# Performance work log

Hardware: AMD Instinct MI355X
Metric: run time of the kernel (lower is better)

## Reference

```python
import jax, jax.numpy as jnp
import numpy as np

N = 50000
E = 800000
IN_FEAT = 256
HIDDEN = 256
NUM_CLASS = 10
NUM_GRAPHS = 512
LAYERS = 2


def setup_inputs() -> dict:
    key = jax.random.key(0)
    ks = jax.random.split(key, 10)
    x = jax.random.normal(ks[0], (N, IN_FEAT), dtype=jnp.float32)
    edge_index = jax.random.randint(ks[1], (2, E), 0, N, dtype=jnp.int32)
    batch = jnp.sort(jax.random.randint(ks[2], (N,), 0, NUM_GRAPHS, dtype=jnp.int32))
    s_in = 1.0 / np.sqrt(IN_FEAT)
    s_h = 1.0 / np.sqrt(HIDDEN)
    enc_W = jax.random.uniform(ks[3], (IN_FEAT, HIDDEN), jnp.float32, -s_in, s_in)
    enc_b = jax.random.uniform(ks[4], (HIDDEN,), jnp.float32, -s_in, s_in)
    conv_W = jax.random.uniform(ks[5], (LAYERS, HIDDEN, HIDDEN), jnp.float32, -s_h, s_h)
    conv_b = jax.random.uniform(ks[6], (LAYERS, HIDDEN), jnp.float32, -s_h, s_h)
    out_W = jax.random.uniform(ks[7], (HIDDEN, NUM_CLASS), jnp.float32, -s_h, s_h)
    out_b = jax.random.uniform(ks[8], (NUM_CLASS,), jnp.float32, -s_h, s_h)
    return {"x": x, "edge_index": edge_index, "batch": batch,
            "enc_W": enc_W, "enc_b": enc_b,
            "conv_W": conv_W, "conv_b": conv_b,
            "out_W": out_W, "out_b": out_b}


def _gcn_conv(x, row, col, deg_norm_edge, W, b):
    # PyG GCNConv: linear transform, then normalized scatter-add aggregation.
    h = x @ W                                   # [N, H]
    msg = h[row] * deg_norm_edge[:, None]       # [E+N, H] gather + scale
    out = jax.ops.segment_sum(msg, col, num_segments=N)  # scatter-add
    return out + b


def reference(x, edge_index, batch, enc_W, enc_b, conv_W, conv_b, out_W, out_b):
    # self-loops appended once (same structure every layer)
    loops = jnp.arange(N, dtype=edge_index.dtype)
    row = jnp.concatenate([edge_index[0], loops])  # source
    col = jnp.concatenate([edge_index[1], loops])  # target
    deg = jax.ops.segment_sum(jnp.ones_like(col, dtype=x.dtype), col, num_segments=N)
    dinv = jnp.where(deg > 0, jax.lax.rsqrt(deg), 0.0)
    norm = dinv[row] * dinv[col]                # symmetric GCN normalization per edge

    h = x @ enc_W + enc_b
    for i in range(LAYERS):
        h = jax.nn.relu(_gcn_conv(h, row, col, norm, conv_W[i], conv_b[i]))

    # global_mean_pool over `batch` segment ids
    sums = jax.ops.segment_sum(h, batch, num_segments=NUM_GRAPHS)
    cnts = jax.ops.segment_sum(jnp.ones((N,), dtype=h.dtype), batch, num_segments=NUM_GRAPHS)
    pooled = sums / jnp.maximum(cnts, 1.0)[:, None]

    # dropout is identity in eval mode
    return pooled @ out_W + out_b
```

## Files before the change

kernel.cpp:

```cpp
#include <hip/hip_runtime.h>

#define NN 50000
#define NE 800000
#define HD 256
#define NG 512
#define NC 10
#define SCAN_B ((NN + 255) / 256)
#define REP 8
#define GEMM_G ((NN + 31) / 32)
#define EDGE_G ((NE + 255) / 256)

typedef unsigned short u16;
typedef unsigned char u8;
typedef short v8s __attribute__((ext_vector_type(8)));
typedef float v4f __attribute__((ext_vector_type(4)));
typedef float v2f __attribute__((ext_vector_type(2)));
typedef u16 v4u __attribute__((ext_vector_type(4)));

static __device__ __forceinline__ float bf2f(u16 u) {
    return __uint_as_float(((unsigned)u) << 16);
}
static __device__ __forceinline__ u16 f2bf(float f) {
    unsigned u = __float_as_uint(f);
    unsigned r = (u + 0x7fffu + ((u >> 16) & 1u)) >> 16;
    return (u16)r;
}
static __device__ __forceinline__ int clampi(int v, int lo, int hi) {
    return min(max(v, lo), hi);
}
static __device__ __forceinline__ float ldf(const void* p, size_t i, int isbf) {
    return isbf ? bf2f(((const u16*)p)[i]) : ((const float*)p)[i];
}

static __device__ __forceinline__ u8 f32_to_fp8(float f) {
#if __has_builtin(__builtin_amdgcn_cvt_pk_fp8_f32)
    int r = __builtin_amdgcn_cvt_pk_fp8_f32(f, f, 0, false);
    return (u8)(r & 0xff);
#else
    float a = fabsf(f);
    unsigned s = (__float_as_uint(f) >> 31) << 7;
    if (a < 0.0009765625f) return (u8)s;
    a = fminf(a, 448.f);
    if (a < 0.015625f) {
        int m = (int)(a * 512.f + 0.5f);
        return (u8)(s | min(m, 7));
    }
    unsigned u = __float_as_uint(a);
    unsigned r = u + 0x0007FFFFu + ((u >> 20) & 1u);
    int e = (int)(r >> 23) - 127 + 7;
    if (e > 15) return (u8)(s | 0x7E);
    unsigned m = (r >> 20) & 7u;
    return (u8)(s | ((unsigned)e << 3) | m);
#endif
}
static __device__ __forceinline__ v4f fp8x4_to_f32(unsigned v) {
#if __has_builtin(__builtin_amdgcn_cvt_pk_f32_fp8)
    v2f lo = __builtin_amdgcn_cvt_pk_f32_fp8(v, false);
    v2f hi = __builtin_amdgcn_cvt_pk_f32_fp8(v, true);
    return (v4f){lo[0], lo[1], hi[0], hi[1]};
#else
    v4f o;
#pragma unroll
    for (int j = 0; j < 4; j++) {
        unsigned b = (v >> (8 * j)) & 0xffu;
        unsigned e = (b >> 3) & 15u, m = b & 7u;
        float val = e ? __uint_as_float(((e + 120u) << 23) | (m << 20))
                      : (float)m * 0.001953125f;
        o[j] = (b & 0x80u) ? -val : val;
    }
    return o;
#endif
}

__global__ void k_detect(const u16* __restrict__ xu, int* __restrict__ mode) {
    __shared__ int cnt;
    if (threadIdx.x == 0) cnt = 0;
    __syncthreads();
    int bad = 0;
    for (int i = threadIdx.x; i < 4096; i += 256) {
        float v = bf2f(xu[2 * i]);
        float av = fabsf(v);
        if (av > 100.f || (av < 1e-3f && av != 0.f)) bad++;
    }
    atomicAdd(&cnt, bad);
    __syncthreads();
    if (threadIdx.x == 0) mode[0] = (cnt > 1024) ? 0 : 1;
}

__global__ void k_prep(const void* __restrict__ enc_W, const void* __restrict__ conv_W,
                       const void* __restrict__ enc_b, const void* __restrict__ conv_b,
                       const void* __restrict__ out_b,
                       u16* __restrict__ Wp, float* __restrict__ biasf,
                       const int* __restrict__ modep) {
    int md = modep[0];
    int b = blockIdx.x;
    if (b < 768) {
        int wi = b >> 8;
        int n = b & 255, k = threadIdx.x;
        const void* W = (wi == 0) ? enc_W : conv_W;
        size_t off = (wi == 0) ? 0 : (size_t)(wi - 1) * HD * HD;
        int nt = n >> 4, m = n & 15;
        int ks = k >> 5, q = (k >> 3) & 3, j = k & 7;
        size_t idx = ((((size_t)nt * 8 + ks) * 64) + q * 16 + m) * 8 + j;
        Wp[(size_t)wi * HD * HD + idx] = f2bf(ldf(W, off + (size_t)k * HD + n, md));
    } else {
        for (int j = threadIdx.x; j < 768 + NC; j += 256) {
            float v = (j < 256) ? ldf(enc_b, j, md)
                    : (j < 768) ? ldf(conv_b, j - 256, md)
                                : ldf(out_b, j - 768, md);
            biasf[j] = v;
        }
    }
}

static __device__ __forceinline__ void edges_body(
        int i, const int* __restrict__ ecol, const int* __restrict__ batch,
        int* __restrict__ deg_r, int* __restrict__ gptr) {
    int r = (i >> 8) & (REP - 1);
    if (i < NE) atomicAdd(&deg_r[r * NN + clampi(ecol[i], 0, NN - 1)], 1);
    if (i < NN) {
        int b = clampi(batch[i], 0, NG - 1);
        int bp = (i == 0) ? -1 : clampi(batch[i - 1], 0, NG - 1);
        for (int g = bp + 1; g <= b; g++) gptr[g] = i;
        if (i == NN - 1)
            for (int g = b + 1; g <= NG; g++) gptr[g] = NN;
    }
}

static __device__ __forceinline__ void scatter_body(
        int i, const int* __restrict__ row, const int* __restrict__ col,
        const int* __restrict__ cptr, const int* __restrict__ offc,
        int* __restrict__ fill_r, int* __restrict__ csrc) {
    int r = (i >> 8) & (REP - 1);
    if (i < NE) {
        int c = clampi(col[i], 0, NN - 1);
        int rw = clampi(row[i], 0, NN - 1);
        int pos = cptr[c] + offc[r * NN + c] + atomicAdd(&fill_r[r * NN + c], 1);
        if (pos >= 0 && pos < NE) csrc[pos] = rw;
    }
}

static __device__ __forceinline__ void gemm_body(
        int bid, u16* As, const void* __restrict__ A, const u16* __restrict__ Wp,
        const float* __restrict__ biasf, const float* __restrict__ dinvp,
        void* __restrict__ out, int M, int hasBias, int outFp8, int amode) {
    int tid = threadIdx.x;
    int wave = tid >> 6;
    int lane = tid & 63;
    int row0 = bid * 32;
    if (row0 >= M) return;
    int m = lane & 15, q = lane >> 4;

#pragma unroll
    for (int it = 0; it < 4; it++) {
        int fb = it * 4 + wave;
        int mt = fb >> 3, ks = fb & 7;
        int row = min(row0 + mt * 16 + m, M - 1);
        int colE = ks * 32 + q * 8;
        v8s v;
        if (amode) {
            v = *(const v8s*)((const u16*)A + (size_t)row * HD + colE);
        } else {
            const float* af = (const float*)A + (size_t)row * HD + colE;
            v4f x0 = *(const v4f*)af;
            v4f x1 = *(const v4f*)(af + 4);
            v[0] = (short)f2bf(x0[0]); v[1] = (short)f2bf(x0[1]);
            v[2] = (short)f2bf(x0[2]); v[3] = (short)f2bf(x0[3]);
            v[4] = (short)f2bf(x1[0]); v[5] = (short)f2bf(x1[1]);
            v[6] = (short)f2bf(x1[2]); v[7] = (short)f2bf(x1[3]);
        }
        *(v8s*)&As[((size_t)fb * 64 + lane) * 8] = v;
    }
    __syncthreads();

    v4f acc[2][4];
#pragma unroll
    for (int i = 0; i < 2; i++)
#pragma unroll
        for (int j = 0; j < 4; j++) acc[i][j] = (v4f){0.f, 0.f, 0.f, 0.f};

    const u16* wp = Wp + (size_t)wave * 4 * 8 * 64 * 8;

#pragma unroll
    for (int ks = 0; ks < 8; ks++) {
        v8s bfr[4];
#pragma unroll
        for (int nt = 0; nt < 4; nt++)
            bfr[nt] = *(const v8s*)(wp + ((size_t)(nt * 8 + ks) * 64 + lane) * 8);
        v8s a[2];
#pragma unroll
        for (int mt = 0; mt < 2; mt++)
            a[mt] = *(const v8s*)&As[((size_t)(mt * 8 + ks) * 64 + lane) * 8];
#pragma unroll
        for (int mt = 0; mt < 2; mt++)
#pragma unroll
            for (int nt = 0; nt < 4; nt++)
                acc[mt][nt] = __builtin_amdgcn_mfma_f32_16x16x32_bf16(
                    a[mt], bfr[nt], acc[mt][nt], 0, 0, 0);
    }
    if (outFp8) {
#pragma unroll
        for (int mt = 0; mt < 2; mt++) {
            float dv[4];
#pragma unroll
            for (int r = 0; r < 4; r++) {
                int orow = row0 + mt * 16 + q * 4 + r;
                dv[r] = (orow < M) ? dinvp[orow] * 32.f : 0.f;
            }
#pragma unroll
            for (int nt = 0; nt < 4; nt++) {
                int ocol = wave * 64 + nt * 16 + m;
#pragma unroll
                for (int r = 0; r < 4; r++) {
                    int orow = row0 + mt * 16 + q * 4 + r;
                    if (orow < M)
                        ((u8*)out)[(size_t)orow * HD + ocol] =
                            f32_to_fp8(acc[mt][nt][r] * dv[r]);
                }
            }
        }
    } else {
#pragma unroll
        for (int mt = 0; mt < 2; mt++) {
#pragma unroll
            for (int nt = 0; nt < 4; nt++) {
                int ocol = wave * 64 + nt * 16 + m;
                float badd = hasBias ? biasf[ocol] : 0.f;
#pragma unroll
                for (int r = 0; r < 4; r++) {
                    int orow = row0 + mt * 16 + q * 4 + r;
                    if (orow < M)
                        ((u16*)out)[(size_t)orow * HD + ocol] =
                            f2bf(acc[mt][nt][r] + badd);
                }
            }
        }
    }
}

__global__ __launch_bounds__(256) void k_gemm(
        const void* __restrict__ A, const u16* __restrict__ Wp,
        const float* __restrict__ biasf, const float* __restrict__ dinvp,
        void* __restrict__ out, int M, int hasBias, int outFp8,
        const int* __restrict__ modep, int forceBf) {
    __shared__ u16 As[16 * 64 * 8];
    gemm_body(blockIdx.x, As, A, Wp, biasf, dinvp, out, M, hasBias, outFp8,
              forceBf ? 1 : modep[0]);
}

__global__ __launch_bounds__(256) void k_edges(
        const int* __restrict__ ecol, const int* __restrict__ batch,
        int* __restrict__ deg_r, int* __restrict__ gptr) {
    edges_body(blockIdx.x * 256 + threadIdx.x, ecol, batch, deg_r, gptr);
}

__global__ __launch_bounds__(256) void k_scatter(
        const int* __restrict__ row, const int* __restrict__ col,
        const int* __restrict__ cptr, const int* __restrict__ offc,
        int* __restrict__ fill_r, int* __restrict__ csrc) {
    scatter_body(blockIdx.x * 256 + threadIdx.x, row, col, cptr, offc, fill_r, csrc);
}

__global__ __launch_bounds__(256) void k_gemm_edges(
        const void* __restrict__ A, const u16* __restrict__ Wp,
        const float* __restrict__ biasf, void* __restrict__ out,
        int M, int hasBias, const int* __restrict__ modep, int forceBf,
        const int* __restrict__ ecol, const int* __restrict__ batch,
        int* __restrict__ deg_r, int* __restrict__ gptr) {
    __shared__ u16 As[16 * 64 * 8];
    if (blockIdx.x < GEMM_G) {
        gemm_body(blockIdx.x, As, A, Wp, biasf, nullptr, out, M, hasBias, 0,
                  forceBf ? 1 : modep[0]);
    } else {
        edges_body((blockIdx.x - GEMM_G) * 256 + threadIdx.x, ecol, batch, deg_r, gptr);
    }
}

__global__ __launch_bounds__(256) void k_gemm_scatter(
        const void* __restrict__ A, const u16* __restrict__ Wp,
        const float* __restrict__ dinvp, void* __restrict__ out,
        int M, const int* __restrict__ modep,
        const int* __restrict__ erow, const int* __restrict__ ecol,
        const int* __restrict__ cptr, const int* __restrict__ offc,
        int* __restrict__ fill_r, int* __restrict__ csrc) {
    __shared__ u16 As[16 * 64 * 8];
    if (blockIdx.x < GEMM_G) {
        gemm_body(blockIdx.x, As, A, Wp, nullptr, dinvp, out, M, 0, 1, 1);
    } else {
        scatter_body((blockIdx.x - GEMM_G) * 256 + threadIdx.x,
                     erow, ecol, cptr, offc, fill_r, csrc);
    }
}

__global__ __launch_bounds__(256) void k_scan_blk(
        const int* __restrict__ deg_r, int* __restrict__ offc,
        int* __restrict__ degtot, float* __restrict__ dinv,
        int* __restrict__ bsum) {
    int t = threadIdx.x;
    int i = blockIdx.x * 256 + t;
    int d = 0;
    if (i < NN) {
        int run = 0;
#pragma unroll
        for (int r = 0; r < REP; r++) {
            int v = deg_r[r * NN + i];
            offc[r * NN + i] = run;
            run += v;
        }
        d = run;
        degtot[i] = d;
        dinv[i] = rsqrtf((float)(d + 1));
    }
    __shared__ int sh[256];
    sh[t] = d;
    __syncthreads();
    for (int off = 128; off > 0; off >>= 1) {
        if (t < off) sh[t] += sh[t + off];
        __syncthreads();
    }
    if (t == 0) bsum[blockIdx.x] = sh[0];
}

__global__ __launch_bounds__(256) void k_scan_top(
        const int* __restrict__ bsum, int* __restrict__ boff) {
    __shared__ int sh[256];
    int t = threadIdx.x;
    int v = (t < SCAN_B) ? bsum[t] : 0;
    sh[t] = v;
    __syncthreads();
    for (int off = 1; off < 256; off <<= 1) {
        int x = (t >= off) ? sh[t - off] : 0;
        __syncthreads();
        sh[t] += x;
        __syncthreads();
    }
    if (t < SCAN_B) boff[t] = sh[t] - v;
}

__global__ __launch_bounds__(256) void k_scan_fin(
        const int* __restrict__ degtot, const int* __restrict__ boff,
        int* __restrict__ cptr) {
    int t = threadIdx.x;
    int i = blockIdx.x * 256 + t;
    int d = (i < NN) ? degtot[i] : 0;
    __shared__ int sh[256];
    sh[t] = d;
    __syncthreads();
    for (int off = 1; off < 256; off <<= 1) {
        int x = (t >= off) ? sh[t - off] : 0;
        __syncthreads();
        sh[t] += x;
        __syncthreads();
    }
    int excl = sh[t] - d + boff[blockIdx.x];
    if (i < NN) cptr[i] = excl;
    if (i == NN - 1) cptr[NN] = excl + d;
}

__global__ __launch_bounds__(256) void k_aggregate(
        const u8* __restrict__ t, const int* __restrict__ cptr,
        const int* __restrict__ csrc, const float* __restrict__ dinv,
        const float* __restrict__ biasf, u16* __restrict__ out) {
    int wave = threadIdx.x >> 6;
    int lane = threadIdx.x & 63;
    int node = blockIdx.x * 4 + wave;
    if (node >= NN) return;
    int f0 = lane * 4;
    const u8* tf = t + f0;

    unsigned sv = *(const unsigned*)(tf + (size_t)node * HD);
    v4f sd = fp8x4_to_f32(sv);
    float a0 = sd[0], a1 = sd[1], a2 = sd[2], a3 = sd[3];

    int e0 = cptr[node], e1 = cptr[node + 1];
    e1 = clampi(e1, 0, NE);
    e0 = clampi(e0, 0, e1);
    int e = e0;
    for (; e + 8 <= e1; e += 8) {
        int s[8];
#pragma unroll
        for (int j = 0; j < 8; j++) s[j] = clampi(csrc[e + j], 0, NN - 1);
        unsigned rv[8];
#pragma unroll
        for (int j = 0; j < 8; j++) rv[j] = *(const unsigned*)(tf + (size_t)s[j] * HD);
#pragma unroll
        for (int j = 0; j < 8; j++) {
            v4f d = fp8x4_to_f32(rv[j]);
            a0 += d[0]; a1 += d[1]; a2 += d[2]; a3 += d[3];
        }
    }
    for (; e + 4 <= e1; e += 4) {
        int s0 = clampi(csrc[e], 0, NN - 1);
        int s1 = clampi(csrc[e + 1], 0, NN - 1);
        int s2 = clampi(csrc[e + 2], 0, NN - 1);
        int s3 = clampi(csrc[e + 3], 0, NN - 1);
        unsigned r0 = *(const unsigned*)(tf + (size_t)s0 * HD);
        unsigned r1 = *(const unsigned*)(tf + (size_t)s1 * HD);
        unsigned r2 = *(const unsigned*)(tf + (size_t)s2 * HD);
        unsigned r3 = *(const unsigned*)(tf + (size_t)s3 * HD);
        v4f d0 = fp8x4_to_f32(r0), d1 = fp8x4_to_f32(r1);
        v4f d2 = fp8x4_to_f32(r2), d3 = fp8x4_to_f32(r3);
        a0 += d0[0] + d1[0] + d2[0] + d3[0];
        a1 += d0[1] + d1[1] + d2[1] + d3[1];
        a2 += d0[2] + d1[2] + d2[2] + d3[2];
        a3 += d0[3] + d1[3] + d2[3] + d3[3];
    }
    for (; e < e1; e++) {
        int src = clampi(csrc[e], 0, NN - 1);
        unsigned rv = *(const unsigned*)(tf + (size_t)src * HD);
        v4f d = fp8x4_to_f32(rv);
        a0 += d[0]; a1 += d[1]; a2 += d[2]; a3 += d[3];
    }
    float sc = dinv[node] * 0.03125f;
    v4f b = *(const v4f*)(biasf + f0);
    a0 = fmaxf(a0 * sc + b[0], 0.f);
    a1 = fmaxf(a1 * sc + b[1], 0.f);
    a2 = fmaxf(a2 * sc + b[2], 0.f);
    a3 = fmaxf(a3 * sc + b[3], 0.f);
    v4u o = {f2bf(a0), f2bf(a1), f2bf(a2), f2bf(a3)};
    *(v4u*)(out + (size_t)node * HD + f0) = o;
}

__global__ __launch_bounds__(256) void k_head(
        const u16* __restrict__ h, const int* __restrict__ gptr,
        const void* __restrict__ W, const float* __restrict__ biasf,
        void* __restrict__ outv, const int* __restrict__ modep) {
    int md = modep[0];
    int g = blockIdx.x, f = threadIdx.x;
    int hi = clampi(gptr[g + 1], 0, NN);
    int lo = clampi(gptr[g], 0, hi);
    float s0 = 0.f, s1 = 0.f, s2 = 0.f, s3 = 0.f;
    int i = lo;
    for (; i + 4 <= hi; i += 4) {
        s0 += bf2f(h[(size_t)i * HD + f]);
        s1 += bf2f(h[(size_t)(i + 1) * HD + f]);
        s2 += bf2f(h[(size_t)(i + 2) * HD + f]);
        s3 += bf2f(h[(size_t)(i + 3) * HD + f]);
    }
    for (; i < hi; i++) s0 += bf2f(h[(size_t)i * HD + f]);
    __shared__ float ps[256];
    ps[f] = ((s0 + s1) + (s2 + s3)) / fmaxf((float)(hi - lo), 1.0f);
    __syncthreads();
    if (threadIdx.x < 64) {
        int lane = threadIdx.x;
        float acc[NC];
#pragma unroll
        for (int c = 0; c < NC; c++) acc[c] = 0.f;
        for (int k = lane; k < HD; k += 64) {
            float p = ps[k];
#pragma unroll
            for (int c = 0; c < NC; c++) acc[c] += p * ldf(W, (size_t)k * NC + c, md);
        }
#pragma unroll
        for (int c = 0; c < NC; c++) {
            for (int off = 32; off > 0; off >>= 1)
                acc[c] += __shfl_down(acc[c], off, 64);
        }
        if (lane == 0) {
#pragma unroll
            for (int c = 0; c < NC; c++) {
                float vv = acc[c] + biasf[768 + c];
                if (md) ((u16*)outv)[g * NC + c] = f2bf(vv);
                else    ((float*)outv)[g * NC + c] = vv;
            }
        }
    }
}

extern "C" void kernel_launch(void* const* d_in, const int* in_sizes, int n_in,
                              void* d_out, int out_size, void* d_ws, size_t ws_size,
                              hipStream_t stream) {
    const void* x      = d_in[0];
    const int*  ei     = (const int*)d_in[1];
    const int*  batch  = (const int*)d_in[2];
    const void* enc_W  = d_in[3];
    const void* enc_b  = d_in[4];
    const void* conv_W = d_in[5];
    const void* conv_b = d_in[6];
    const void* out_W  = d_in[7];
    const void* out_b  = d_in[8];

    char* w = (char*)d_ws;
    auto alloc = [&](size_t b) { char* p = w; w += (b + 255) & ~(size_t)255; return p; };
    int*   mode   = (int*)alloc(256);
    float* dinv   = (float*)alloc(NN * 4);
    int*   cptr   = (int*)alloc((NN + 1) * 4);
    int*   gptr   = (int*)alloc((NG + 1) * 4);
    int*   bsum   = (int*)alloc(SCAN_B * 4);
    int*   boff   = (int*)alloc(SCAN_B * 4);
    int*   csrc   = (int*)alloc((size_t)NE * 4);
    u16*   Wp     = (u16*)alloc((size_t)3 * HD * HD * 2);
    float* biasf  = (float*)alloc(778 * 4);
    u16*   hbuf   = (u16*)alloc((size_t)NN * HD * 2);
    size_t scratch_need = ((size_t)3 * REP * NN + NN) * 4 + 512;
    size_t used = (size_t)(w - (char*)d_ws);
    bool fused = (used + scratch_need <= ws_size);
    int* deg_r = fused ? (int*)alloc(scratch_need) : (int*)hbuf;
    int* fill_r = deg_r + REP * NN;
    int* offc   = fill_r + REP * NN;
    int* degtot = offc + REP * NN;
    u8* tbuf = (u8*)d_in[0];

    const int* erow = ei;
    const int* ecol = ei + NE;

    hipMemsetAsync(deg_r, 0, (size_t)2 * REP * NN * 4, stream);
    k_detect<<<1, 256, 0, stream>>>((const u16*)x, mode);
    k_prep<<<769, 256, 0, stream>>>(enc_W, conv_W, enc_b, conv_b, out_b, Wp, biasf, mode);

    if (fused) {
        k_gemm_edges<<<GEMM_G + EDGE_G, 256, 0, stream>>>(
            x, Wp, biasf, hbuf, NN, 1, mode, 0, ecol, batch, deg_r, gptr);
        k_scan_blk<<<SCAN_B, 256, 0, stream>>>(deg_r, offc, degtot, dinv, bsum);
        k_scan_top<<<1, 256, 0, stream>>>(bsum, boff);
        k_scan_fin<<<SCAN_B, 256, 0, stream>>>(degtot, boff, cptr);
        k_gemm_scatter<<<GEMM_G + EDGE_G, 256, 0, stream>>>(
            hbuf, Wp + (size_t)HD * HD, dinv, tbuf, NN, mode,
            erow, ecol, cptr, offc, fill_r, csrc);
    } else {
        k_edges<<<EDGE_G, 256, 0, stream>>>(ecol, batch, deg_r, gptr);
        k_scan_blk<<<SCAN_B, 256, 0, stream>>>(deg_r, offc, degtot, dinv, bsum);
        k_scan_top<<<1, 256, 0, stream>>>(bsum, boff);
        k_scan_fin<<<SCAN_B, 256, 0, stream>>>(degtot, boff, cptr);
        k_scatter<<<EDGE_G, 256, 0, stream>>>(erow, ecol, cptr, offc, fill_r, csrc);
        k_gemm<<<GEMM_G, 256, 0, stream>>>(x, Wp, biasf, nullptr, hbuf,
                                           NN, 1, 0, mode, 0);
        k_gemm<<<GEMM_G, 256, 0, stream>>>(hbuf, Wp + (size_t)HD * HD, nullptr,
                                           dinv, tbuf, NN, 0, 1, mode, 1);
    }
    k_aggregate<<<(NN + 3) / 4, 256, 0, stream>>>(tbuf, cptr, csrc, dinv,
                                                  biasf + 256, hbuf);
    k_gemm<<<GEMM_G, 256, 0, stream>>>(hbuf, Wp + (size_t)2 * HD * HD, nullptr,
                                       dinv, tbuf, NN, 0, 1, mode, 1);
    k_aggregate<<<(NN + 3) / 4, 256, 0, stream>>>(tbuf, cptr, csrc, dinv,
                                                  biasf + 256 + HD, hbuf);
    k_head<<<NG, 256, 0, stream>>>(hbuf, gptr, out_W, biasf, d_out, mode);
}
```

Measured before the change: 314.2 us.

## Store hidden activations in FP8 and interleave GEMM with edge blocks

The intermediate hidden buffer switches from bf16 to fp8: the encoder GEMM and aggregation kernels write fp8, and the following GEMMs and the pooling head read fp8, halving activation traffic. The fused GEMM+edges and GEMM+scatter launches now interleave one GEMM block with two edge blocks instead of placing all GEMM blocks first, so the two kinds of work mix across CUs. This adds precision loss on activations, including the encoder output before the first convolution, which risks exceeding tolerance.

New measurement: 324.6 us. +3.3%, slower.

```diff
diff --git a/kernel.cpp b/kernel.cpp
--- a/kernel.cpp
+++ b/kernel.cpp
@@ -9,6 +9,7 @@
 #define REP 8
 #define GEMM_G ((NN + 31) / 32)
 #define EDGE_G ((NE + 255) / 256)
+#define FUSE_G (3 * GEMM_G)
 
 typedef unsigned short u16;
 typedef unsigned char u8;
@@ -53,6 +54,17 @@
     return (u8)(s | ((unsigned)e << 3) | m);
 #endif
 }
+static __device__ __forceinline__ unsigned f32x4_to_fp8x4(float a0, float a1,
+                                                          float a2, float a3) {
+#if __has_builtin(__builtin_amdgcn_cvt_pk_fp8_f32)
+    int p = __builtin_amdgcn_cvt_pk_fp8_f32(a0, a1, 0, false);
+    p = __builtin_amdgcn_cvt_pk_fp8_f32(a2, a3, p, true);
+    return (unsigned)p;
+#else
+    return (unsigned)f32_to_fp8(a0) | ((unsigned)f32_to_fp8(a1) << 8)
+         | ((unsigned)f32_to_fp8(a2) << 16) | ((unsigned)f32_to_fp8(a3) << 24);
+#endif
+}
 static __device__ __forceinline__ v4f fp8x4_to_f32(unsigned v) {
 #if __has_builtin(__builtin_amdgcn_cvt_pk_f32_fp8)
     v2f lo = __builtin_amdgcn_cvt_pk_f32_fp8(v, false);
@@ -70,6 +82,12 @@
     }
     return o;
 #endif
+}
+static __device__ __forceinline__ float fp8_to_f32(u8 b) {
+    unsigned e = (b >> 3) & 15u, m = b & 7u;
+    float val = e ? __uint_as_float(((e + 120u) << 23) | (m << 20))
+                  : (float)m * 0.001953125f;
+    return (b & 0x80u) ? -val : val;
 }
 
 __global__ void k_detect(const u16* __restrict__ xu, int* __restrict__ mode) {
@@ -143,7 +161,7 @@
 static __device__ __forceinline__ void gemm_body(
         int bid, u16* As, const void* __restrict__ A, const u16* __restrict__ Wp,
         const float* __restrict__ biasf, const float* __restrict__ dinvp,
-        void* __restrict__ out, int M, int hasBias, int outFp8, int amode) {
+        void* __restrict__ out, int M, int outKind, int amode) {
     int tid = threadIdx.x;
     int wave = tid >> 6;
     int lane = tid & 63;
@@ -158,9 +176,9 @@
         int row = min(row0 + mt * 16 + m, M - 1);
         int colE = ks * 32 + q * 8;
         v8s v;
-        if (amode) {
+        if (amode == 1) {
             v = *(const v8s*)((const u16*)A + (size_t)row * HD + colE);
-        } else {
+        } else if (amode == 0) {
             const float* af = (const float*)A + (size_t)row * HD + colE;
             v4f x0 = *(const v4f*)af;
             v4f x1 = *(const v4f*)(af + 4);
@@ -168,6 +186,15 @@
             v[2] = (short)f2bf(x0[2]); v[3] = (short)f2bf(x0[3]);
             v[4] = (short)f2bf(x1[0]); v[5] = (short)f2bf(x1[1]);
             v[6] = (short)f2bf(x1[2]); v[7] = (short)f2bf(x1[3]);
+        } else {
+            const u8* af = (const u8*)A + (size_t)row * HD + colE;
+            unsigned lo = *(const unsigned*)af;
+            unsigned hi = *(const unsigned*)(af + 4);
+            v4f x0 = fp8x4_to_f32(lo), x1 = fp8x4_to_f32(hi);
+            v[0] = (short)f2bf(x0[0]); v[1] = (short)f2bf(x0[1]);
+            v[2] = (short)f2bf(x0[2]); v[3] = (short)f2bf(x0[3]);
+            v[4] = (short)f2bf(x1[0]); v[5] = (short)f2bf(x1[1]);
+            v[6] = (short)f2bf(x1[2]); v[7] = (short)f2bf(x1[3]);
         }
         *(v8s*)&As[((size_t)fb * 64 + lane) * 8] = v;
     }
@@ -198,7 +225,7 @@
                 acc[mt][nt] = __builtin_amdgcn_mfma_f32_16x16x32_bf16(
                     a[mt], bfr[nt], acc[mt][nt], 0, 0, 0);
     }
-    if (outFp8) {
+    if (outKind == 1) {
 #pragma unroll
         for (int mt = 0; mt < 2; mt++) {
             float dv[4];
@@ -225,13 +252,13 @@
 #pragma unroll
             for (int nt = 0; nt < 4; nt++) {
                 int ocol = wave * 64 + nt * 16 + m;
-                float badd = hasBias ? biasf[ocol] : 0.f;
+                float badd = biasf ? biasf[ocol] : 0.f;
 #pragma unroll
                 for (int r = 0; r < 4; r++) {
                     int orow = row0 + mt * 16 + q * 4 + r;
                     if (orow < M)
-                        ((u16*)out)[(size_t)orow * HD + ocol] =
-                            f2bf(acc[mt][nt][r] + badd);
+                        ((u8*)out)[(size_t)orow * HD + ocol] =
+                            f32_to_fp8(acc[mt][nt][r] + badd);
                 }
             }
         }
@@ -241,11 +268,11 @@
 __global__ __launch_bounds__(256) void k_gemm(
         const void* __restrict__ A, const u16* __restrict__ Wp,
         const float* __restrict__ biasf, const float* __restrict__ dinvp,
-        void* __restrict__ out, int M, int hasBias, int outFp8,
-        const int* __restrict__ modep, int forceBf) {
+        void* __restrict__ out, int M, int outKind, int amodeSel,
+        const int* __restrict__ modep) {
     __shared__ u16 As[16 * 64 * 8];
-    gemm_body(blockIdx.x, As, A, Wp, biasf, dinvp, out, M, hasBias, outFp8,
-              forceBf ? 1 : modep[0]);
+    int amode = (amodeSel < 0) ? modep[0] : amodeSel;
+    gemm_body(blockIdx.x, As, A, Wp, biasf, dinvp, out, M, outKind, amode);
 }
 
 __global__ __launch_bounds__(256) void k_edges(
@@ -264,31 +291,32 @@
 __global__ __launch_bounds__(256) void k_gemm_edges(
         const void* __restrict__ A, const u16* __restrict__ Wp,
         const float* __restrict__ biasf, void* __restrict__ out,
-        int M, int hasBias, const int* __restrict__ modep, int forceBf,
+        int M, const int* __restrict__ modep,
         const int* __restrict__ ecol, const int* __restrict__ batch,
         int* __restrict__ deg_r, int* __restrict__ gptr) {
     __shared__ u16 As[16 * 64 * 8];
-    if (blockIdx.x < GEMM_G) {
-        gemm_body(blockIdx.x, As, A, Wp, biasf, nullptr, out, M, hasBias, 0,
-                  forceBf ? 1 : modep[0]);
+    int r3 = blockIdx.x % 3, q3 = blockIdx.x / 3;
+    if (r3 == 0) {
+        gemm_body(q3, As, A, Wp, biasf, nullptr, out, M, 2, modep[0]);
     } else {
-        edges_body((blockIdx.x - GEMM_G) * 256 + threadIdx.x, ecol, batch, deg_r, gptr);
+        int ei = (q3 * 2 + (r3 - 1)) * 256 + threadIdx.x;
+        edges_body(ei, ecol, batch, deg_r, gptr);
     }
 }
 
 __global__ __launch_bounds__(256) void k_gemm_scatter(
         const void* __restrict__ A, const u16* __restrict__ Wp,
-        const float* __restrict__ dinvp, void* __restrict__ out,
-        int M, const int* __restrict__ modep,
+        const float* __restrict__ dinvp, void* __restrict__ out, int M,
         const int* __restrict__ erow, const int* __restrict__ ecol,
         const int* __restrict__ cptr, const int* __restrict__ offc,
         int* __restrict__ fill_r, int* __restrict__ csrc) {
     __shared__ u16 As[16 * 64 * 8];
-    if (blockIdx.x < GEMM_G) {
-        gemm_body(blockIdx.x, As, A, Wp, nullptr, dinvp, out, M, 0, 1, 1);
+    int r3 = blockIdx.x % 3, q3 = blockIdx.x / 3;
+    if (r3 == 0) {
+        gemm_body(q3, As, A, Wp, nullptr, dinvp, out, M, 1, 2);
     } else {
-        scatter_body((blockIdx.x - GEMM_G) * 256 + threadIdx.x,
-                     erow, ecol, cptr, offc, fill_r, csrc);
+        int ei = (q3 * 2 + (r3 - 1)) * 256 + threadIdx.x;
+        scatter_body(ei, erow, ecol, cptr, offc, fill_r, csrc);
     }
 }
 
@@ -360,7 +388,7 @@
 __global__ __launch_bounds__(256) void k_aggregate(
         const u8* __restrict__ t, const int* __restrict__ cptr,
         const int* __restrict__ csrc, const float* __restrict__ dinv,
-        const float* __restrict__ biasf, u16* __restrict__ out) {
+        const float* __restrict__ biasf, u8* __restrict__ out) {
     int wave = threadIdx.x >> 6;
     int lane = threadIdx.x & 63;
     int node = blockIdx.x * 4 + wave;
@@ -417,12 +445,11 @@
     a1 = fmaxf(a1 * sc + b[1], 0.f);
     a2 = fmaxf(a2 * sc + b[2], 0.f);
     a3 = fmaxf(a3 * sc + b[3], 0.f);
-    v4u o = {f2bf(a0), f2bf(a1), f2bf(a2), f2bf(a3)};
-    *(v4u*)(out + (size_t)node * HD + f0) = o;
+    *(unsigned*)(out + (size_t)node * HD + f0) = f32x4_to_fp8x4(a0, a1, a2, a3);
 }
 
 __global__ __launch_bounds__(256) void k_head(
-        const u16* __restrict__ h, const int* __restrict__ gptr,
+        const u8* __restrict__ h, const int* __restrict__ gptr,
         const void* __restrict__ W, const float* __restrict__ biasf,
         void* __restrict__ outv, const int* __restrict__ modep) {
     int md = modep[0];
@@ -432,12 +459,12 @@
     float s0 = 0.f, s1 = 0.f, s2 = 0.f, s3 = 0.f;
     int i = lo;
     for (; i + 4 <= hi; i += 4) {
-        s0 += bf2f(h[(size_t)i * HD + f]);
-        s1 += bf2f(h[(size_t)(i + 1) * HD + f]);
-        s2 += bf2f(h[(size_t)(i + 2) * HD + f]);
-        s3 += bf2f(h[(size_t)(i + 3) * HD + f]);
-    }
-    for (; i < hi; i++) s0 += bf2f(h[(size_t)i * HD + f]);
+        s0 += fp8_to_f32(h[(size_t)i * HD + f]);
+        s1 += fp8_to_f32(h[(size_t)(i + 1) * HD + f]);
+        s2 += fp8_to_f32(h[(size_t)(i + 2) * HD + f]);
+        s3 += fp8_to_f32(h[(size_t)(i + 3) * HD + f]);
+    }
+    for (; i < hi; i++) s0 += fp8_to_f32(h[(size_t)i * HD + f]);
     __shared__ float ps[256];
     ps[f] = ((s0 + s1) + (s2 + s3)) / fmaxf((float)(hi - lo), 1.0f);
     __syncthreads();
@@ -491,7 +518,7 @@
     int*   csrc   = (int*)alloc((size_t)NE * 4);
     u16*   Wp     = (u16*)alloc((size_t)3 * HD * HD * 2);
     float* biasf  = (float*)alloc(778 * 4);
-    u16*   hbuf   = (u16*)alloc((size_t)NN * HD * 2);
+    u8*    hbuf   = (u8*)alloc((size_t)NN * HD);
     size_t scratch_need = ((size_t)3 * REP * NN + NN) * 4 + 512;
     size_t used = (size_t)(w - (char*)d_ws);
     bool fused = (used + scratch_need <= ws_size);
@@ -509,13 +536,13 @@
     k_prep<<<769, 256, 0, stream>>>(enc_W, conv_W, enc_b, conv_b, out_b, Wp, biasf, mode);
 
     if (fused) {
-        k_gemm_edges<<<GEMM_G + EDGE_G, 256, 0, stream>>>(
-            x, Wp, biasf, hbuf, NN, 1, mode, 0, ecol, batch, deg_r, gptr);
+        k_gemm_edges<<<FUSE_G, 256, 0, stream>>>(
+            x, Wp, biasf, hbuf, NN, mode, ecol, batch, deg_r, gptr);
         k_scan_blk<<<SCAN_B, 256, 0, stream>>>(deg_r, offc, degtot, dinv, bsum);
         k_scan_top<<<1, 256, 0, stream>>>(bsum, boff);
         k_scan_fin<<<SCAN_B, 256, 0, stream>>>(degtot, boff, cptr);
-        k_gemm_scatter<<<GEMM_G + EDGE_G, 256, 0, stream>>>(
-            hbuf, Wp + (size_t)HD * HD, dinv, tbuf, NN, mode,
+        k_gemm_scatter<<<FUSE_G, 256, 0, stream>>>(
+            hbuf, Wp + (size_t)HD * HD, dinv, tbuf, NN,
             erow, ecol, cptr, offc, fill_r, csrc);
     } else {
         k_edges<<<EDGE_G, 256, 0, stream>>>(ecol, batch, deg_r, gptr);
@@ -524,14 +551,14 @@
         k_scan_fin<<<SCAN_B, 256, 0, stream>>>(degtot, boff, cptr);
         k_scatter<<<EDGE_G, 256, 0, stream>>>(erow, ecol, cptr, offc, fill_r, csrc);
         k_gemm<<<GEMM_G, 256, 0, stream>>>(x, Wp, biasf, nullptr, hbuf,
-                                           NN, 1, 0, mode, 0);
+                                           NN, 2, -1, mode);
         k_gemm<<<GEMM_G, 256, 0, stream>>>(hbuf, Wp + (size_t)HD * HD, nullptr,
-                                           dinv, tbuf, NN, 0, 1, mode, 1);
+                                           dinv, tbuf, NN, 1, 2, mode);
     }
     k_aggregate<<<(NN + 3) / 4, 256, 0, stream>>>(tbuf, cptr, csrc, dinv,
                                                   biasf + 256, hbuf);
     k_gemm<<<GEMM_G, 256, 0, stream>>>(hbuf, Wp + (size_t)2 * HD * HD, nullptr,
-                                       dinv, tbuf, NN, 0, 1, mode, 1);
+                                       dinv, tbuf, NN, 1, 2, mode);
     k_aggregate<<<(NN + 3) / 4, 256, 0, stream>>>(tbuf, cptr, csrc, dinv,
                                                   biasf + 256 + HD, hbuf);
     k_head<<<NG, 256, 0, stream>>>(hbuf, gptr, out_W, biasf, d_out, mode);
```
